# Kernel optimization log

Measured on AMD Instinct MI355X. Metric: run time of the kernel, lower is better.

Reference implementation:

```python
import jax, jax.numpy as jnp
import numpy as np

B, K, D, TPE, PPE, HEADS = 8, 128, 128, 64, 64, 8


def setup_inputs() -> dict:
    key = jax.random.key(0)
    ks = jax.random.split(key, 16)
    rn = lambda i, s: jax.random.normal(ks[i], s, dtype=jnp.float32)
    w = lambda i, s: rn(i, s) * 0.05
    z = lambda n: jnp.zeros((n,), jnp.float32)
    return {
        "v_f": rn(0, (B, K, D)),
        "e_f": rn(1, (B, K * K, D)),
        "p_pe": rn(2, (B, K, PPE)),
        "t_pe": rn(3, (B, TPE)),
        "W_vpe": w(4, (D + PPE + TPE, D)), "b_vpe": z(D),
        "W_epe": w(5, (D + TPE, D)), "b_epe": z(D),
        "W_ev1": w(6, (D + 2 * D, D)), "b_ev1": z(D),
        "W_ev2": w(7, (D, D)), "b_ev2": z(D),
        "W_q": w(8, (D, D)), "b_q": z(D),
        "W_k": w(9, (D, D)), "b_k": z(D),
        "W_self": w(10, (D, D)), "b_self": z(D),
        "W_out": w(11, (2 * D, D)), "b_out": z(D),
    }


def reference(v_f, e_f, p_pe, t_pe, W_vpe, b_vpe, W_epe, b_epe, W_ev1, b_ev1,
              W_ev2, b_ev2, W_q, b_q, W_k, b_k, W_self, b_self, W_out, b_out):
    silu = jax.nn.silu
    Bv, Kv, _ = v_f.shape
    t_dim = t_pe.shape[-1]
    # PE binding MLPs
    t_v = jnp.broadcast_to(t_pe[:, None, :], (Bv, Kv, t_dim))
    v = silu(jnp.concatenate([v_f, p_pe, t_v], -1) @ W_vpe + b_vpe)  # [B,K,D]
    t_e = jnp.broadcast_to(t_pe[:, None, :], (Bv, Kv * Kv, t_dim))
    e = silu(jnp.concatenate([e_f, t_e], -1) @ W_epe + b_epe)        # [B,K*K,D]
    Dv = v.shape[-1]
    # pairwise node features + edge feature -> edge value MLP
    e_mtx = e.reshape(Bv, Kv, Kv, -1)
    ev = jnp.concatenate([
        jnp.broadcast_to(v[:, :, None, :], (Bv, Kv, Kv, Dv)),
        jnp.broadcast_to(v[:, None, :, :], (Bv, Kv, Kv, Dv)),
        e_mtx], -1)                                                   # [B,K,K,3D]
    e_value = silu(ev @ W_ev1 + b_ev1) @ W_ev2 + b_ev2                # [B,K,K,E]
    E = e_value.shape[-1]
    G = E // HEADS
    # grouped-head elementwise-QK attention, softmax over neighbor axis (2)
    q = v @ W_q + b_q
    k = v @ W_k + b_k
    scores = (q[:, :, None, :] * k[:, None, :, :]).reshape(Bv, Kv, Kv, G, HEADS)
    scores = scores.sum(-1) / np.float32(np.sqrt(HEADS * 3.0))        # [B,K,K,G]
    atten = jax.nn.softmax(scores, axis=2)
    agg = (atten[..., None] * e_value.reshape(Bv, Kv, Kv, G, HEADS)).sum(2)
    agg = agg.reshape(Bv, Kv, E)
    vf = agg + silu(v @ W_self + b_self)
    pool = jnp.broadcast_to(vf.max(axis=1, keepdims=True), vf.shape)
    v_out = silu(jnp.concatenate([vf, pool], -1) @ W_out + b_out)     # [B,K,Vout]
    return v_out, e_value.reshape(Bv, Kv * Kv, E)
```

## Files before the change

### kernel.cpp

```cpp
#include <hip/hip_runtime.h>
#include <hip/hip_bf16.h>


typedef __attribute__((ext_vector_type(8)))  short bh8;
typedef __attribute__((ext_vector_type(16))) float f16v;
typedef __attribute__((ext_vector_type(4)))  float f4v;

__device__ __forceinline__ unsigned short f2bf(float f) {
  unsigned u = __builtin_bit_cast(unsigned, f);
  u += 0x7fffu + ((u >> 16) & 1u);
  return (unsigned short)(u >> 16);
}
__device__ __forceinline__ float silu_f(float x) {
  float e = __builtin_amdgcn_exp2f(x * -1.44269504088896f);
  return x * __builtin_amdgcn_rcpf(1.f + e);
}
__device__ __forceinline__ bh8 cvt8(f4v x, f4v y) {
  bh8 a;
  a[0] = (short)f2bf(x[0]); a[1] = (short)f2bf(x[1]);
  a[2] = (short)f2bf(x[2]); a[3] = (short)f2bf(x[3]);
  a[4] = (short)f2bf(y[0]); a[5] = (short)f2bf(y[1]);
  a[6] = (short)f2bf(y[2]); a[7] = (short)f2bf(y[3]);
  return a;
}
typedef const __attribute__((address_space(1))) unsigned int gq_t;
typedef __attribute__((address_space(3))) unsigned int lq_t;
__device__ __forceinline__ void gload_lds16(const void* g, void* l) {
  __builtin_amdgcn_global_load_lds((gq_t*)g, (lq_t*)l, 16, 0, 0);
}
__device__ __forceinline__ unsigned fkey(float x) {
  unsigned u = __builtin_bit_cast(unsigned, x);
  return u ^ (((unsigned)((int)u >> 31)) | 0x80000000u);
}
__device__ __forceinline__ float funkey(unsigned key) {
  unsigned u = (key & 0x80000000u) ? (key ^ 0x80000000u) : ~key;
  return __builtin_bit_cast(float, u);
}

__device__ __forceinline__ void wfrag_work(const float* __restrict__ W,
                                           short* __restrict__ dst, int kdim,
                                           int blk, int nblk) {
  int ksteps = kdim >> 4;
  int total  = kdim * 128;
  for (int idx = blk * 256 + threadIdx.x; idx < total; idx += nblk * 256) {
    int jj = idx & 7;
    int l  = (idx >> 3) & 63;
    int rest = idx >> 9;
    int ks = rest % ksteps;
    int ni = rest / ksteps;
    int n  = ni * 32 + (l & 31);
    int kk = ks * 16 + ((l >> 5) << 3) + jj;
    dst[idx] = (short)f2bf(W[kk * 128 + n]);
  }
}

__global__ __launch_bounds__(256) void k_front(
    const float* __restrict__ W_epe, short* __restrict__ wf1,
    const float* __restrict__ W_ev1, short* __restrict__ wf2,
    const float* __restrict__ W_ev2, short* __restrict__ wf3,
    const float* __restrict__ tpe, const float* __restrict__ bepe,
    float* __restrict__ tc, unsigned* __restrict__ poolU,
    const float* __restrict__ vfeat, const float* __restrict__ ppe,
    const float* __restrict__ Wv, const float* __restrict__ bv,
    const float* __restrict__ Wq, const float* __restrict__ bq,
    const float* __restrict__ Wk, const float* __restrict__ bk,
    const float* __restrict__ Ws, const float* __restrict__ bs,
    const float* __restrict__ We, const float* __restrict__ be,
    unsigned short* __restrict__ vb16, float* __restrict__ q,
    float* __restrict__ kb, float* __restrict__ sa, float* __restrict__ evi) {
  const int blk = blockIdx.x;
  if (blk < 260) {
    if (blk < 64)       wfrag_work(W_epe, wf1, 128, blk, 64);
    else if (blk < 192) wfrag_work(W_ev1 + 128 * 128, wf2, 256, blk - 64, 128);
    else if (blk < 256) wfrag_work(W_ev2, wf3, 128, blk - 192, 64);
    else {
      int t = threadIdx.x;
      int b = (blk - 256) * 2 + (t >> 7);
      int n = t & 127;
      float a = bepe[n];
      for (int k2 = 0; k2 < 64; ++k2)
        a += tpe[b * 64 + k2] * W_epe[(128 + k2) * 128 + n];
      tc[b * 128 + n] = a;
    }
    return;
  }
  if (blk == 260) {
    for (int j = threadIdx.x; j < 1024; j += 256) poolU[j] = 0u;
    return;
  }
  __shared__ float x[2][256];
  __shared__ float par[2][2][128];
  __shared__ float xv[2][128];
  const int r0 = (blk - 261) * 2;
  const int b  = r0 >> 7;
  const int t  = threadIdx.x;
  const int c  = t & 127;
  const int hf = t >> 7;
  #pragma unroll
  for (int rr = 0; rr < 2; ++rr) {
    int row = r0 + rr;
    x[rr][t] = (t < 128) ? vfeat[row * 128 + t]
             : (t < 192) ? ppe[row * 64 + (t - 128)]
                         : tpe[b * 64 + (t - 192)];
  }
  __syncthreads();
  {
    float a0 = 0.f, a1 = 0.f;
    const int k0 = hf * 128;
    for (int k4 = k0; k4 < k0 + 128; k4 += 4) {
      f4v x0 = *(const f4v*)&x[0][k4];
      f4v x1 = *(const f4v*)&x[1][k4];
      #pragma unroll
      for (int u = 0; u < 4; ++u) {
        float wv = Wv[(k4 + u) * 128 + c];
        a0 += x0[u] * wv; a1 += x1[u] * wv;
      }
    }
    par[hf][0][c] = a0; par[hf][1][c] = a1;
  }
  __syncthreads();
  if (hf == 0) {
    const float bvv = bv[c];
    #pragma unroll
    for (int rr = 0; rr < 2; ++rr) {
      float s = silu_f(par[0][rr][c] + par[1][rr][c] + bvv);
      vb16[(r0 + rr) * 128 + c] = f2bf(s);
      xv[rr][c] = s;
    }
  }
  __syncthreads();
  const float* WA = hf ? Ws : Wq;
  const float* WB = hf ? We : Wk;
  const float  ba = hf ? bs[c] : bq[c];
  const float  bb = hf ? be[c] : bk[c];
  float aA[2] = {ba, ba}, aB[2] = {bb, bb};
  for (int k4 = 0; k4 < 128; k4 += 4) {
    f4v x0 = *(const f4v*)&xv[0][k4];
    f4v x1 = *(const f4v*)&xv[1][k4];
    #pragma unroll
    for (int u = 0; u < 4; ++u) {
      float wa = WA[(k4 + u) * 128 + c];
      float wb = WB[(k4 + u) * 128 + c];
      aA[0] += x0[u] * wa; aA[1] += x1[u] * wa;
      aB[0] += x0[u] * wb; aB[1] += x1[u] * wb;
    }
  }
  if (hf == 0) {
    #pragma unroll
    for (int rr = 0; rr < 2; ++rr) {
      q[(r0 + rr) * 128 + c]  = aA[rr];
      kb[(r0 + rr) * 128 + c] = aB[rr];
    }
  } else {
    #pragma unroll
    for (int rr = 0; rr < 2; ++rr) {
      sa[(r0 + rr) * 128 + c]  = silu_f(aA[rr]);
      evi[(r0 + rr) * 128 + c] = aB[rr];
    }
  }
}

__global__ __launch_bounds__(256) void k_atten(
    const float* __restrict__ q, const float* __restrict__ kmat,
    float* __restrict__ atten) {
  __shared__ float qr[2][128];
  __shared__ float s[2][128][17];
  __shared__ float red[2][8][17];
  __shared__ float gmax[2][16];
  __shared__ float gsum[2][16];
  const int tid = threadIdx.x;
  const int hi  = tid >> 7;
  const int tt  = tid & 127;
  const int bi  = blockIdx.x * 2 + hi;
  const int b   = bi >> 7;
  qr[hi][tt] = q[(size_t)bi * 128 + tt];
  __syncthreads();
  const float sc = 0.20412414523193154f;
  float loc[16];
  const float* krow = kmat + (size_t)(b * 128 + tt) * 128;
  #pragma unroll
  for (int g = 0; g < 16; ++g) {
    f4v k0 = *(const f4v*)&krow[g * 8];
    f4v k1 = *(const f4v*)&krow[g * 8 + 4];
    float a = 0.f;
    #pragma unroll
    for (int h = 0; h < 4; ++h)
      a += qr[hi][g * 8 + h] * k0[h] + qr[hi][g * 8 + 4 + h] * k1[h];
    loc[g] = a * sc;
    s[hi][tt][g] = loc[g];
  }
  __syncthreads();
  { int g = tt & 15, c = tt >> 4;
    float m = -1e30f;
    for (int j2 = c * 16; j2 < c * 16 + 16; ++j2) m = fmaxf(m, s[hi][j2][g]);
    red[hi][c][g] = m; }
  __syncthreads();
  if (tt < 16) {
    float m = red[hi][0][tt];
    #pragma unroll
    for (int c = 1; c < 8; ++c) m = fmaxf(m, red[hi][c][tt]);
    gmax[hi][tt] = m;
  }
  __syncthreads();
  #pragma unroll
  for (int g = 0; g < 16; ++g) {
    loc[g] = __builtin_amdgcn_exp2f((loc[g] - gmax[hi][g]) * 1.44269504088896f);
    s[hi][tt][g] = loc[g];
  }
  __syncthreads();
  { int g = tt & 15, c = tt >> 4;
    float m = 0.f;
    for (int j2 = c * 16; j2 < c * 16 + 16; ++j2) m += s[hi][j2][g];
    red[hi][c][g] = m; }
  __syncthreads();
  if (tt < 16) {
    float m = 0.f;
    #pragma unroll
    for (int c = 0; c < 8; ++c) m += red[hi][c][tt];
    gsum[hi][tt] = m;
  }
  __syncthreads();
  float* ab = atten + (size_t)bi * 2048 + (size_t)tt * 16;
  #pragma unroll
  for (int g = 0; g < 16; ++g) ab[g] = loc[g] * __builtin_amdgcn_rcpf(gsum[hi][g]);
}

__global__ __launch_bounds__(256) void k_edge(
    const float* __restrict__ ef, const unsigned short* __restrict__ vb,
    const short* __restrict__ wf1, const short* __restrict__ wf2,
    const short* __restrict__ wf3, const float* __restrict__ tc,
    const float* __restrict__ evic, const float* __restrict__ bev2,
    const float* __restrict__ atten, const float* __restrict__ sab,
    float* __restrict__ oute, float* __restrict__ vfb,
    unsigned* __restrict__ poolU) {
  __shared__ __align__(16) unsigned short wbuf0[4096];
  __shared__ __align__(16) unsigned short wbuf1[4096];
  __shared__ __align__(16) unsigned short hbuf[128 * 136];
  const int bi  = ((blockIdx.x & 7) << 7) | (blockIdx.x >> 3);
  const int b   = bi >> 7;
  const int tid = threadIdx.x;
  const int w   = tid >> 6;
  const int l   = tid & 63;
  const int row = w * 32 + (l & 31);
  const int kh  = (l >> 5) << 3;
  const int cb  = l & 31;
  const int rb  = w * 32 + ((l >> 5) << 2);

  const float* efr = ef + (size_t)(bi * 128 + row) * 128;
  const unsigned short* vj = vb + (size_t)(b * 128 + row) * 128;

  auto stage2 = [&](const short* wfp, int KST, int kc, unsigned short* dstb) {
    #pragma unroll
    for (int it = 0; it < 2; ++it) {
      int g  = it * 4 + w;
      int ni = g & 3, kso = g >> 2;
      const short* src = wfp + ((size_t)(ni * KST + kc * 2 + kso) * 64 + l) * 8;
      gload_lds16(src, dstb + g * 512);
    }
  };
  f16v acc[4];
  auto compute2 = [&](const unsigned short* ws2, bh8 aa, bh8 ab2) {
    #pragma unroll
    for (int ni = 0; ni < 4; ++ni) {
      bh8 b0 = *(const bh8*)&ws2[ni * 512 + l * 8];
      acc[ni] = __builtin_amdgcn_mfma_f32_32x32x16_bf16(aa, b0, acc[ni], 0, 0, 0);
    }
    #pragma unroll
    for (int ni = 0; ni < 4; ++ni) {
      bh8 b1 = *(const bh8*)&ws2[(4 + ni) * 512 + l * 8];
      acc[ni] = __builtin_amdgcn_mfma_f32_32x32x16_bf16(ab2, b1, acc[ni], 0, 0, 0);
    }
  };
  auto ldAef = [&](int t) -> bh8 {
    const float* p = efr + t * 16 + kh;
    f4v x0 = *(const f4v*)p;
    f4v x1 = *(const f4v*)(p + 4);
    return cvt8(x0, x1);
  };

  #pragma unroll
  for (int it = 0; it < 8; ++it) {
    int s = it * 4 + w;
    gload_lds16(wf1 + ((size_t)s * 64 + l) * 8, hbuf + s * 512);
  }
  stage2(wf2, 16, 0, wbuf0);
  stage2(wf2, 16, 1, wbuf1);

  float tin[4], ein[4];
  #pragma unroll
  for (int ni = 0; ni < 4; ++ni) {
    tin[ni] = tc[b * 128 + ni * 32 + cb];
    ein[ni] = evic[bi * 128 + ni * 32 + cb];
  }
  #pragma unroll
  for (int ni = 0; ni < 4; ++ni)
    #pragma unroll
    for (int r = 0; r < 16; ++r) acc[ni][r] = tin[ni];

  bh8 a0c = ldAef(0), a1c = ldAef(1);
  __syncthreads();

  #pragma unroll
  for (int p2 = 0; p2 < 4; ++p2) {
    bh8 a0n, a1n;
    if (p2 < 3) { a0n = ldAef(2 * p2 + 2); a1n = ldAef(2 * p2 + 3); }
    #pragma unroll
    for (int ni = 0; ni < 4; ++ni) {
      bh8 b0 = *(const bh8*)&hbuf[(ni * 8 + 2 * p2) * 512 + l * 8];
      acc[ni] = __builtin_amdgcn_mfma_f32_32x32x16_bf16(a0c, b0, acc[ni], 0, 0, 0);
    }
    #pragma unroll
    for (int ni = 0; ni < 4; ++ni) {
      bh8 b1 = *(const bh8*)&hbuf[(ni * 8 + 2 * p2 + 1) * 512 + l * 8];
      acc[ni] = __builtin_amdgcn_mfma_f32_32x32x16_bf16(a1c, b1, acc[ni], 0, 0, 0);
    }
    if (p2 < 3) { a0c = a0n; a1c = a1n; }
  }
  __syncthreads();

  #pragma unroll
  for (int ni = 0; ni < 4; ++ni) {
    int n = ni * 32 + cb;
    #pragma unroll
    for (int r = 0; r < 16; ++r) {
      int rj = rb + (r & 3) + ((r >> 2) << 3);
      hbuf[rj * 136 + n] = f2bf(silu_f(acc[ni][r]));
      acc[ni][r] = ein[ni];
    }
  }
  a0c = *(const bh8*)(vj + kh);
  a1c = *(const bh8*)(vj + 16 + kh);

  #pragma unroll
  for (int c2 = 0; c2 < 8; ++c2) {
    bh8 a0n, a1n;
    if (c2 < 7) {
      const int t0 = 10 + 2 * c2, t1 = t0 + 1;
      a0n = (t0 < 16) ? *(const bh8*)(vj + (t0 - 8) * 16 + kh)
                      : *(const bh8*)&hbuf[row * 136 + (t0 - 16) * 16 + kh];
      a1n = (t1 < 16) ? *(const bh8*)(vj + (t1 - 8) * 16 + kh)
                      : *(const bh8*)&hbuf[row * 136 + (t1 - 16) * 16 + kh];
    }
    compute2((c2 & 1) ? wbuf1 : wbuf0, a0c, a1c);
    if (c2 < 7) { a0c = a0n; a1c = a1n; }
    __syncthreads();
    if (c2 + 2 < 8)       stage2(wf2, 16, c2 + 2, (c2 & 1) ? wbuf1 : wbuf0);
    else if (c2 + 2 < 12) stage2(wf3, 8, c2 + 2 - 8, (c2 & 1) ? wbuf1 : wbuf0);
  }

  #pragma unroll
  for (int ni = 0; ni < 4; ++ni) {
    int n = ni * 32 + cb;
    #pragma unroll
    for (int r = 0; r < 16; ++r) {
      int rj = rb + (r & 3) + ((r >> 2) << 3);
      hbuf[rj * 136 + n] = f2bf(silu_f(acc[ni][r]));
      acc[ni][r] = 0.f;
    }
  }
  a0c = *(const bh8*)&hbuf[row * 136 + kh];
  a1c = *(const bh8*)&hbuf[row * 136 + 16 + kh];

  #pragma unroll
  for (int c3 = 0; c3 < 4; ++c3) {
    bh8 a0n, a1n;
    if (c3 < 3) {
      a0n = *(const bh8*)&hbuf[row * 136 + (2 * c3 + 2) * 16 + kh];
      a1n = *(const bh8*)&hbuf[row * 136 + (2 * c3 + 3) * 16 + kh];
    }
    compute2((c3 & 1) ? wbuf1 : wbuf0, a0c, a1c);
    if (c3 < 3) { a0c = a0n; a1c = a1n; }
    __syncthreads();
    if (c3 + 2 < 4) stage2(wf3, 8, c3 + 2, (c3 & 1) ? wbuf1 : wbuf0);
  }

  #pragma unroll
  for (int ni = 0; ni < 4; ++ni) {
    int n = ni * 32 + cb;
    float bv = bev2[n];
    #pragma unroll
    for (int r = 0; r < 16; ++r) {
      int rj = rb + (r & 3) + ((r >> 2) << 3);
      acc[ni][r] += bv;
      oute[(size_t)(bi * 128 + rj) * 128 + n] = acc[ni][r];
    }
  }

  __syncthreads();
  float* attf = (float*)hbuf;
  float* aggl = attf + 2048;
  const float* ap = atten + (size_t)bi * 2048;
  #pragma unroll
  for (int u = 0; u < 8; ++u) {
    int idx = u * 256 + tid;
    float v = ap[idx];
    int j2 = idx >> 4, g = idx & 15;
    attf[j2 * 16 + (g & 3) * 4 + (g >> 2)] = v;
  }
  float sav = 0.f;
  if (tid < 128) sav = sab[(size_t)bi * 128 + tid];
  __syncthreads();
  float p0 = 0.f, p1 = 0.f, p2 = 0.f, p3 = 0.f;
  const int gl = (l & 31) >> 3;
  #pragma unroll
  for (int r = 0; r < 16; ++r) {
    int rj = rb + (r & 3) + ((r >> 2) << 3);
    f4v av = *(const f4v*)&attf[rj * 16 + gl * 4];
    p0 += av[0] * acc[0][r]; p1 += av[1] * acc[1][r];
    p2 += av[2] * acc[2][r]; p3 += av[3] * acc[3][r];
  }
  p0 += __shfl_xor(p0, 32); p1 += __shfl_xor(p1, 32);
  p2 += __shfl_xor(p2, 32); p3 += __shfl_xor(p3, 32);
  if (l < 32) {
    aggl[w * 128 +  0 + l] = p0;
    aggl[w * 128 + 32 + l] = p1;
    aggl[w * 128 + 64 + l] = p2;
    aggl[w * 128 + 96 + l] = p3;
  }
  __syncthreads();
  if (tid < 128) {
    float vf = aggl[tid] + aggl[128 + tid] + aggl[256 + tid] + aggl[384 + tid] + sav;
    vfb[(size_t)bi * 128 + tid] = vf;
    atomicMax(&poolU[b * 128 + tid], fkey(vf));
  }
}

__global__ __launch_bounds__(256) void k_out(
    const float* __restrict__ vfb, const unsigned* __restrict__ poolU,
    const float* __restrict__ W, const float* __restrict__ bias,
    float* __restrict__ vout) {
  __shared__ float x[2][256];
  __shared__ float par[2][2][128];
  const int r0 = blockIdx.x * 2;
  const int b  = r0 >> 7;
  const int t  = threadIdx.x;
  const int c  = t & 127;
  const int hf = t >> 7;
  #pragma unroll
  for (int rr = 0; rr < 2; ++rr)
    x[rr][t] = (t < 128) ? vfb[(r0 + rr) * 128 + t]
                         : funkey(poolU[b * 128 + (t - 128)]);
  __syncthreads();
  {
    float a0 = 0.f, a1 = 0.f;
    const int k0 = hf * 128;
    for (int k4 = k0; k4 < k0 + 128; k4 += 4) {
      f4v x0 = *(const f4v*)&x[0][k4];
      f4v x1 = *(const f4v*)&x[1][k4];
      #pragma unroll
      for (int u = 0; u < 4; ++u) {
        float wv = W[(k4 + u) * 128 + c];
        a0 += x0[u] * wv; a1 += x1[u] * wv;
      }
    }
    par[hf][0][c] = a0; par[hf][1][c] = a1;
  }
  __syncthreads();
  if (hf == 0) {
    const float bvv = bias[c];
    #pragma unroll
    for (int rr = 0; rr < 2; ++rr)
      vout[(r0 + rr) * 128 + c] = silu_f(par[0][rr][c] + par[1][rr][c] + bvv);
  }
}

extern "C" void kernel_launch(void* const* d_in, const int* in_sizes, int n_in,
                              void* d_out, int out_size, void* d_ws, size_t ws_size,
                              hipStream_t stream) {
  const float* v_f    = (const float*)d_in[0];
  const float* e_f    = (const float*)d_in[1];
  const float* p_pe   = (const float*)d_in[2];
  const float* t_pe   = (const float*)d_in[3];
  const float* W_vpe  = (const float*)d_in[4];
  const float* b_vpe  = (const float*)d_in[5];
  const float* W_epe  = (const float*)d_in[6];
  const float* b_epe  = (const float*)d_in[7];
  const float* W_ev1  = (const float*)d_in[8];
  const float* b_ev1  = (const float*)d_in[9];
  const float* W_ev2  = (const float*)d_in[10];
  const float* b_ev2  = (const float*)d_in[11];
  const float* W_q    = (const float*)d_in[12];
  const float* b_q    = (const float*)d_in[13];
  const float* W_k    = (const float*)d_in[14];
  const float* b_k    = (const float*)d_in[15];
  const float* W_self = (const float*)d_in[16];
  const float* b_self = (const float*)d_in[17];
  const float* W_out  = (const float*)d_in[18];
  const float* b_out  = (const float*)d_in[19];

  char* ws = (char*)d_ws;
  unsigned short* vb16  = (unsigned short*)(ws + 0);
  float*          qbuf  = (float*)(ws + 262144);
  float*          kbuf  = (float*)(ws + 786432);
  float*          sabuf = (float*)(ws + 1310720);
  float*          vfbuf = (float*)(ws + 1835008);
  float*          evic  = (float*)(ws + 2359296);
  unsigned*       poolU = (unsigned*)(ws + 2883584);
  float*          tc    = (float*)(ws + 2887680);
  short*          wf1   = (short*)(ws + 2891776);
  short*          wf2   = (short*)(ws + 2924544);
  short*          wf3   = (short*)(ws + 2990080);
  float*          atten = (float*)(ws + 3022848);

  float* v_out = (float*)d_out;
  float* out_e = (float*)d_out + 131072;

  k_front<<<773, 256, 0, stream>>>(W_epe, wf1, W_ev1, wf2, W_ev2, wf3,
                                   t_pe, b_epe, tc, poolU,
                                   v_f, p_pe, W_vpe, b_vpe, W_q, b_q,
                                   W_k, b_k, W_self, b_self, W_ev1, b_ev1,
                                   vb16, qbuf, kbuf, sabuf, evic);
  k_atten<<<512, 256, 0, stream>>>(qbuf, kbuf, atten);
  k_edge<<<1024, 256, 0, stream>>>(e_f, vb16, wf1, wf2, wf3, tc, evic,
                                   b_ev2, atten, sabuf, out_e, vfbuf, poolU);
  k_out<<<512, 256, 0, stream>>>(vfbuf, poolU, W_out, b_out, v_out);
}
```

Baseline: 76.46 us.

## Fuse attention softmax kernel into edge kernel prologue

Removes the separate k_atten launch and computes the per-row grouped softmax at the start of k_edge, using the hbuf shared arena. Attention weights are written to global memory in a pre-transposed layout, then read back directly from global (L1/L2) in the aggregation step instead of being staged through LDS. This saves a kernel launch and an LDS staging pass. In exchange, k_edge gets a serial prologue with many barriers in which only half the threads do work, placed in front of the MFMA pipeline.

```diff
diff --git a/kernel.cpp b/kernel.cpp
--- a/kernel.cpp
+++ b/kernel.cpp
@@ -160,77 +160,13 @@
   }
 }
 
-__global__ __launch_bounds__(256) void k_atten(
-    const float* __restrict__ q, const float* __restrict__ kmat,
-    float* __restrict__ atten) {
-  __shared__ float qr[2][128];
-  __shared__ float s[2][128][17];
-  __shared__ float red[2][8][17];
-  __shared__ float gmax[2][16];
-  __shared__ float gsum[2][16];
-  const int tid = threadIdx.x;
-  const int hi  = tid >> 7;
-  const int tt  = tid & 127;
-  const int bi  = blockIdx.x * 2 + hi;
-  const int b   = bi >> 7;
-  qr[hi][tt] = q[(size_t)bi * 128 + tt];
-  __syncthreads();
-  const float sc = 0.20412414523193154f;
-  float loc[16];
-  const float* krow = kmat + (size_t)(b * 128 + tt) * 128;
-  #pragma unroll
-  for (int g = 0; g < 16; ++g) {
-    f4v k0 = *(const f4v*)&krow[g * 8];
-    f4v k1 = *(const f4v*)&krow[g * 8 + 4];
-    float a = 0.f;
-    #pragma unroll
-    for (int h = 0; h < 4; ++h)
-      a += qr[hi][g * 8 + h] * k0[h] + qr[hi][g * 8 + 4 + h] * k1[h];
-    loc[g] = a * sc;
-    s[hi][tt][g] = loc[g];
-  }
-  __syncthreads();
-  { int g = tt & 15, c = tt >> 4;
-    float m = -1e30f;
-    for (int j2 = c * 16; j2 < c * 16 + 16; ++j2) m = fmaxf(m, s[hi][j2][g]);
-    red[hi][c][g] = m; }
-  __syncthreads();
-  if (tt < 16) {
-    float m = red[hi][0][tt];
-    #pragma unroll
-    for (int c = 1; c < 8; ++c) m = fmaxf(m, red[hi][c][tt]);
-    gmax[hi][tt] = m;
-  }
-  __syncthreads();
-  #pragma unroll
-  for (int g = 0; g < 16; ++g) {
-    loc[g] = __builtin_amdgcn_exp2f((loc[g] - gmax[hi][g]) * 1.44269504088896f);
-    s[hi][tt][g] = loc[g];
-  }
-  __syncthreads();
-  { int g = tt & 15, c = tt >> 4;
-    float m = 0.f;
-    for (int j2 = c * 16; j2 < c * 16 + 16; ++j2) m += s[hi][j2][g];
-    red[hi][c][g] = m; }
-  __syncthreads();
-  if (tt < 16) {
-    float m = 0.f;
-    #pragma unroll
-    for (int c = 0; c < 8; ++c) m += red[hi][c][tt];
-    gsum[hi][tt] = m;
-  }
-  __syncthreads();
-  float* ab = atten + (size_t)bi * 2048 + (size_t)tt * 16;
-  #pragma unroll
-  for (int g = 0; g < 16; ++g) ab[g] = loc[g] * __builtin_amdgcn_rcpf(gsum[hi][g]);
-}
-
 __global__ __launch_bounds__(256) void k_edge(
     const float* __restrict__ ef, const unsigned short* __restrict__ vb,
     const short* __restrict__ wf1, const short* __restrict__ wf2,
     const short* __restrict__ wf3, const float* __restrict__ tc,
     const float* __restrict__ evic, const float* __restrict__ bev2,
-    const float* __restrict__ atten, const float* __restrict__ sab,
+    const float* __restrict__ qbuf, const float* __restrict__ kbuf,
+    float* __restrict__ atten, const float* __restrict__ sab,
     float* __restrict__ oute, float* __restrict__ vfb,
     unsigned* __restrict__ poolU) {
   __shared__ __align__(16) unsigned short wbuf0[4096];
@@ -249,6 +185,77 @@
   const float* efr = ef + (size_t)(bi * 128 + row) * 128;
   const unsigned short* vj = vb + (size_t)(b * 128 + row) * 128;
 
+  {
+    float* arena = (float*)hbuf;
+    float* qr   = arena;
+    float* s    = arena + 128;
+    float* red  = arena + 2304;
+    float* gmax = arena + 2448;
+    float* gsum = arena + 2464;
+    const float sc = 0.20412414523193154f;
+    float loc[16];
+    if (tid < 128) qr[tid] = qbuf[(size_t)bi * 128 + tid];
+    __syncthreads();
+    if (tid < 128) {
+      const float* krow = kbuf + (size_t)(b * 128 + tid) * 128;
+      #pragma unroll
+      for (int g = 0; g < 16; ++g) {
+        f4v k0 = *(const f4v*)&krow[g * 8];
+        f4v k1 = *(const f4v*)&krow[g * 8 + 4];
+        float a = 0.f;
+        #pragma unroll
+        for (int h = 0; h < 4; ++h)
+          a += qr[g * 8 + h] * k0[h] + qr[g * 8 + 4 + h] * k1[h];
+        loc[g] = a * sc;
+        s[tid * 17 + g] = loc[g];
+      }
+    }
+    __syncthreads();
+    if (tid < 128) {
+      int g = tid & 15, cp = tid >> 4;
+      float m = -1e30f;
+      for (int j2 = cp * 16; j2 < cp * 16 + 16; ++j2) m = fmaxf(m, s[j2 * 17 + g]);
+      red[cp * 17 + g] = m;
+    }
+    __syncthreads();
+    if (tid < 16) {
+      float m = red[tid];
+      #pragma unroll
+      for (int cp = 1; cp < 8; ++cp) m = fmaxf(m, red[cp * 17 + tid]);
+      gmax[tid] = m;
+    }
+    __syncthreads();
+    if (tid < 128) {
+      #pragma unroll
+      for (int g = 0; g < 16; ++g) {
+        loc[g] = __builtin_amdgcn_exp2f((loc[g] - gmax[g]) * 1.44269504088896f);
+        s[tid * 17 + g] = loc[g];
+      }
+    }
+    __syncthreads();
+    if (tid < 128) {
+      int g = tid & 15, cp = tid >> 4;
+      float m = 0.f;
+      for (int j2 = cp * 16; j2 < cp * 16 + 16; ++j2) m += s[j2 * 17 + g];
+      red[cp * 17 + g] = m;
+    }
+    __syncthreads();
+    if (tid < 16) {
+      float m = 0.f;
+      #pragma unroll
+      for (int cp = 0; cp < 8; ++cp) m += red[cp * 17 + tid];
+      gsum[tid] = m;
+    }
+    __syncthreads();
+    if (tid < 128) {
+      float* ab = atten + (size_t)bi * 2048;
+      #pragma unroll
+      for (int g = 0; g < 16; ++g)
+        ab[tid * 16 + (g & 3) * 4 + (g >> 2)] = loc[g] * __builtin_amdgcn_rcpf(gsum[g]);
+    }
+    __syncthreads();
+  }
+
   auto stage2 = [&](const short* wfp, int KST, int kc, unsigned short* dstb) {
     #pragma unroll
     for (int it = 0; it < 2; ++it) {
@@ -387,25 +394,16 @@
   }
 
   __syncthreads();
-  float* attf = (float*)hbuf;
-  float* aggl = attf + 2048;
+  float* aggl = (float*)hbuf;
   const float* ap = atten + (size_t)bi * 2048;
-  #pragma unroll
-  for (int u = 0; u < 8; ++u) {
-    int idx = u * 256 + tid;
-    float v = ap[idx];
-    int j2 = idx >> 4, g = idx & 15;
-    attf[j2 * 16 + (g & 3) * 4 + (g >> 2)] = v;
-  }
   float sav = 0.f;
   if (tid < 128) sav = sab[(size_t)bi * 128 + tid];
-  __syncthreads();
   float p0 = 0.f, p1 = 0.f, p2 = 0.f, p3 = 0.f;
   const int gl = (l & 31) >> 3;
   #pragma unroll
   for (int r = 0; r < 16; ++r) {
     int rj = rb + (r & 3) + ((r >> 2) << 3);
-    f4v av = *(const f4v*)&attf[rj * 16 + gl * 4];
+    f4v av = *(const f4v*)&ap[rj * 16 + gl * 4];
     p0 += av[0] * acc[0][r]; p1 += av[1] * acc[1][r];
     p2 += av[2] * acc[2][r]; p3 += av[3] * acc[3][r];
   }
@@ -510,8 +508,8 @@
                                    v_f, p_pe, W_vpe, b_vpe, W_q, b_q,
                                    W_k, b_k, W_self, b_self, W_ev1, b_ev1,
                                    vb16, qbuf, kbuf, sabuf, evic);
-  k_atten<<<512, 256, 0, stream>>>(qbuf, kbuf, atten);
   k_edge<<<1024, 256, 0, stream>>>(e_f, vb16, wf1, wf2, wf3, tc, evic,
-                                   b_ev2, atten, sabuf, out_e, vfbuf, poolU);
+                                   b_ev2, qbuf, kbuf, atten, sabuf,
+                                   out_e, vfbuf, poolU);
   k_out<<<512, 256, 0, stream>>>(vfbuf, poolU, W_out, b_out, v_out);
 }
```

Result: slower. 101.9 us (+33.2%).

## Split k_edge output columns across 8 waves with 512-thread blocks

Applied to the files above, without the earlier changes.

Doubles the k_edge block to 512 threads. Each group of four waves now computes half of the 128 output columns, so every wave holds two MFMA accumulators instead of four. This cuts accumulator register pressure and raises the number of waves per block, which should help hide latency. The cost is that each wave loads the A operand (edge features, node features, hidden) twice across the column groups, and an extra __syncthreads is needed before reading hbuf.

```diff
diff --git a/kernel.cpp b/kernel.cpp
--- a/kernel.cpp
+++ b/kernel.cpp
@@ -5,6 +5,7 @@
 typedef __attribute__((ext_vector_type(8)))  short bh8;
 typedef __attribute__((ext_vector_type(16))) float f16v;
 typedef __attribute__((ext_vector_type(4)))  float f4v;
+typedef __attribute__((ext_vector_type(2)))  float f2v;
 
 __device__ __forceinline__ unsigned short f2bf(float f) {
   unsigned u = __builtin_bit_cast(unsigned, f);
@@ -225,7 +226,7 @@
   for (int g = 0; g < 16; ++g) ab[g] = loc[g] * __builtin_amdgcn_rcpf(gsum[hi][g]);
 }
 
-__global__ __launch_bounds__(256) void k_edge(
+__global__ __launch_bounds__(512) void k_edge(
     const float* __restrict__ ef, const unsigned short* __restrict__ vb,
     const short* __restrict__ wf1, const short* __restrict__ wf2,
     const short* __restrict__ wf3, const float* __restrict__ tc,
@@ -241,34 +242,33 @@
   const int tid = threadIdx.x;
   const int w   = tid >> 6;
   const int l   = tid & 63;
-  const int row = w * 32 + (l & 31);
+  const int wr  = w & 3;
+  const int ch  = w >> 2;
+  const int ni0 = ch * 2;
+  const int row = wr * 32 + (l & 31);
   const int kh  = (l >> 5) << 3;
   const int cb  = l & 31;
-  const int rb  = w * 32 + ((l >> 5) << 2);
+  const int rb  = wr * 32 + ((l >> 5) << 2);
 
   const float* efr = ef + (size_t)(bi * 128 + row) * 128;
   const unsigned short* vj = vb + (size_t)(b * 128 + row) * 128;
 
   auto stage2 = [&](const short* wfp, int KST, int kc, unsigned short* dstb) {
-    #pragma unroll
-    for (int it = 0; it < 2; ++it) {
-      int g  = it * 4 + w;
-      int ni = g & 3, kso = g >> 2;
-      const short* src = wfp + ((size_t)(ni * KST + kc * 2 + kso) * 64 + l) * 8;
-      gload_lds16(src, dstb + g * 512);
-    }
+    int ni = w & 3, kso = w >> 2;
+    gload_lds16(wfp + ((size_t)(ni * KST + kc * 2 + kso) * 64 + l) * 8,
+                dstb + w * 512);
   };
-  f16v acc[4];
+  f16v acc[2];
   auto compute2 = [&](const unsigned short* ws2, bh8 aa, bh8 ab2) {
     #pragma unroll
-    for (int ni = 0; ni < 4; ++ni) {
-      bh8 b0 = *(const bh8*)&ws2[ni * 512 + l * 8];
-      acc[ni] = __builtin_amdgcn_mfma_f32_32x32x16_bf16(aa, b0, acc[ni], 0, 0, 0);
-    }
-    #pragma unroll
-    for (int ni = 0; ni < 4; ++ni) {
-      bh8 b1 = *(const bh8*)&ws2[(4 + ni) * 512 + l * 8];
-      acc[ni] = __builtin_amdgcn_mfma_f32_32x32x16_bf16(ab2, b1, acc[ni], 0, 0, 0);
+    for (int q2 = 0; q2 < 2; ++q2) {
+      bh8 b0 = *(const bh8*)&ws2[(ni0 + q2) * 512 + l * 8];
+      acc[q2] = __builtin_amdgcn_mfma_f32_32x32x16_bf16(aa, b0, acc[q2], 0, 0, 0);
+    }
+    #pragma unroll
+    for (int q2 = 0; q2 < 2; ++q2) {
+      bh8 b1 = *(const bh8*)&ws2[(4 + ni0 + q2) * 512 + l * 8];
+      acc[q2] = __builtin_amdgcn_mfma_f32_32x32x16_bf16(ab2, b1, acc[q2], 0, 0, 0);
     }
   };
   auto ldAef = [&](int t) -> bh8 {
@@ -279,23 +279,23 @@
   };
 
   #pragma unroll
-  for (int it = 0; it < 8; ++it) {
-    int s = it * 4 + w;
+  for (int it = 0; it < 4; ++it) {
+    int s = it * 8 + w;
     gload_lds16(wf1 + ((size_t)s * 64 + l) * 8, hbuf + s * 512);
   }
   stage2(wf2, 16, 0, wbuf0);
   stage2(wf2, 16, 1, wbuf1);
 
-  float tin[4], ein[4];
-  #pragma unroll
-  for (int ni = 0; ni < 4; ++ni) {
-    tin[ni] = tc[b * 128 + ni * 32 + cb];
-    ein[ni] = evic[bi * 128 + ni * 32 + cb];
-  }
-  #pragma unroll
-  for (int ni = 0; ni < 4; ++ni)
-    #pragma unroll
-    for (int r = 0; r < 16; ++r) acc[ni][r] = tin[ni];
+  float tin[2], ein[2];
+  #pragma unroll
+  for (int q2 = 0; q2 < 2; ++q2) {
+    tin[q2] = tc[b * 128 + (ni0 + q2) * 32 + cb];
+    ein[q2] = evic[bi * 128 + (ni0 + q2) * 32 + cb];
+  }
+  #pragma unroll
+  for (int q2 = 0; q2 < 2; ++q2)
+    #pragma unroll
+    for (int r = 0; r < 16; ++r) acc[q2][r] = tin[q2];
 
   bh8 a0c = ldAef(0), a1c = ldAef(1);
   __syncthreads();
@@ -305,27 +305,27 @@
     bh8 a0n, a1n;
     if (p2 < 3) { a0n = ldAef(2 * p2 + 2); a1n = ldAef(2 * p2 + 3); }
     #pragma unroll
-    for (int ni = 0; ni < 4; ++ni) {
-      bh8 b0 = *(const bh8*)&hbuf[(ni * 8 + 2 * p2) * 512 + l * 8];
-      acc[ni] = __builtin_amdgcn_mfma_f32_32x32x16_bf16(a0c, b0, acc[ni], 0, 0, 0);
-    }
-    #pragma unroll
-    for (int ni = 0; ni < 4; ++ni) {
-      bh8 b1 = *(const bh8*)&hbuf[(ni * 8 + 2 * p2 + 1) * 512 + l * 8];
-      acc[ni] = __builtin_amdgcn_mfma_f32_32x32x16_bf16(a1c, b1, acc[ni], 0, 0, 0);
+    for (int q2 = 0; q2 < 2; ++q2) {
+      bh8 b0 = *(const bh8*)&hbuf[((ni0 + q2) * 8 + 2 * p2) * 512 + l * 8];
+      acc[q2] = __builtin_amdgcn_mfma_f32_32x32x16_bf16(a0c, b0, acc[q2], 0, 0, 0);
+    }
+    #pragma unroll
+    for (int q2 = 0; q2 < 2; ++q2) {
+      bh8 b1 = *(const bh8*)&hbuf[((ni0 + q2) * 8 + 2 * p2 + 1) * 512 + l * 8];
+      acc[q2] = __builtin_amdgcn_mfma_f32_32x32x16_bf16(a1c, b1, acc[q2], 0, 0, 0);
     }
     if (p2 < 3) { a0c = a0n; a1c = a1n; }
   }
   __syncthreads();
 
   #pragma unroll
-  for (int ni = 0; ni < 4; ++ni) {
-    int n = ni * 32 + cb;
+  for (int q2 = 0; q2 < 2; ++q2) {
+    int n = (ni0 + q2) * 32 + cb;
     #pragma unroll
     for (int r = 0; r < 16; ++r) {
       int rj = rb + (r & 3) + ((r >> 2) << 3);
-      hbuf[rj * 136 + n] = f2bf(silu_f(acc[ni][r]));
-      acc[ni][r] = ein[ni];
+      hbuf[rj * 136 + n] = f2bf(silu_f(acc[q2][r]));
+      acc[q2][r] = ein[q2];
     }
   }
   a0c = *(const bh8*)(vj + kh);
@@ -349,15 +349,16 @@
   }
 
   #pragma unroll
-  for (int ni = 0; ni < 4; ++ni) {
-    int n = ni * 32 + cb;
+  for (int q2 = 0; q2 < 2; ++q2) {
+    int n = (ni0 + q2) * 32 + cb;
     #pragma unroll
     for (int r = 0; r < 16; ++r) {
       int rj = rb + (r & 3) + ((r >> 2) << 3);
-      hbuf[rj * 136 + n] = f2bf(silu_f(acc[ni][r]));
-      acc[ni][r] = 0.f;
-    }
-  }
+      hbuf[rj * 136 + n] = f2bf(silu_f(acc[q2][r]));
+      acc[q2][r] = 0.f;
+    }
+  }
+  __syncthreads();
   a0c = *(const bh8*)&hbuf[row * 136 + kh];
   a1c = *(const bh8*)&hbuf[row * 136 + 16 + kh];
 
@@ -375,14 +376,14 @@
   }
 
   #pragma unroll
-  for (int ni = 0; ni < 4; ++ni) {
-    int n = ni * 32 + cb;
+  for (int q2 = 0; q2 < 2; ++q2) {
+    int n = (ni0 + q2) * 32 + cb;
     float bv = bev2[n];
     #pragma unroll
     for (int r = 0; r < 16; ++r) {
       int rj = rb + (r & 3) + ((r >> 2) << 3);
-      acc[ni][r] += bv;
-      oute[(size_t)(bi * 128 + rj) * 128 + n] = acc[ni][r];
+      acc[q2][r] += bv;
+      oute[(size_t)(bi * 128 + rj) * 128 + n] = acc[q2][r];
     }
   }
 
@@ -391,8 +392,8 @@
   float* aggl = attf + 2048;
   const float* ap = atten + (size_t)bi * 2048;
   #pragma unroll
-  for (int u = 0; u < 8; ++u) {
-    int idx = u * 256 + tid;
+  for (int u = 0; u < 4; ++u) {
+    int idx = u * 512 + tid;
     float v = ap[idx];
     int j2 = idx >> 4, g = idx & 15;
     attf[j2 * 16 + (g & 3) * 4 + (g >> 2)] = v;
@@ -400,22 +401,19 @@
   float sav = 0.f;
   if (tid < 128) sav = sab[(size_t)bi * 128 + tid];
   __syncthreads();
-  float p0 = 0.f, p1 = 0.f, p2 = 0.f, p3 = 0.f;
+  float p0 = 0.f, p1 = 0.f;
   const int gl = (l & 31) >> 3;
   #pragma unroll
   for (int r = 0; r < 16; ++r) {
     int rj = rb + (r & 3) + ((r >> 2) << 3);
-    f4v av = *(const f4v*)&attf[rj * 16 + gl * 4];
+    f2v av = *(const f2v*)&attf[rj * 16 + gl * 4 + ni0];
     p0 += av[0] * acc[0][r]; p1 += av[1] * acc[1][r];
-    p2 += av[2] * acc[2][r]; p3 += av[3] * acc[3][r];
-  }
-  p0 += __shfl_xor(p0, 32); p1 += __shfl_xor(p1, 32);
-  p2 += __shfl_xor(p2, 32); p3 += __shfl_xor(p3, 32);
+  }
+  p0 += __shfl_xor(p0, 32);
+  p1 += __shfl_xor(p1, 32);
   if (l < 32) {
-    aggl[w * 128 +  0 + l] = p0;
-    aggl[w * 128 + 32 + l] = p1;
-    aggl[w * 128 + 64 + l] = p2;
-    aggl[w * 128 + 96 + l] = p3;
+    aggl[wr * 128 + ni0 * 32 + l]        = p0;
+    aggl[wr * 128 + (ni0 + 1) * 32 + l]  = p1;
   }
   __syncthreads();
   if (tid < 128) {
@@ -511,7 +509,7 @@
                                    W_k, b_k, W_self, b_self, W_ev1, b_ev1,
                                    vb16, qbuf, kbuf, sabuf, evic);
   k_atten<<<512, 256, 0, stream>>>(qbuf, kbuf, atten);
-  k_edge<<<1024, 256, 0, stream>>>(e_f, vb16, wf1, wf2, wf3, tc, evic,
+  k_edge<<<1024, 512, 0, stream>>>(e_f, vb16, wf1, wf2, wf3, tc, evic,
                                    b_ev2, atten, sabuf, out_e, vfbuf, poolU);
   k_out<<<512, 256, 0, stream>>>(vfbuf, poolU, W_out, b_out, v_out);
 }
```

New measurement: 81.04 us. 6.0% more time.
